# Optimization experiments

Hardware: AMD Instinct MI355X
Metric: run time of the kernel (lower is better)

## Reference

```python
import jax, jax.numpy as jnp
import numpy as np

NUM_HEADS = 16
BLOCK = 64  # block_size = min(64, N)

def setup_inputs() -> dict:
    key = jax.random.key(0)
    k0, k1, k2 = jax.random.split(key, 3)
    B, N, C = 2, 2048, 1024
    x = jax.random.normal(k0, (B, N, C), dtype=jnp.float32)
    w_qkv = jax.random.normal(k1, (3 * C, C), dtype=jnp.float32) * 0.02  # torch Linear weight [out,in]
    w_proj = jax.random.normal(k2, (C, C), dtype=jnp.float32) * 0.02
    b_proj = jnp.zeros((C,), dtype=jnp.float32)
    return {"x": x, "w_qkv": w_qkv, "w_proj": w_proj, "b_proj": b_proj}

def reference(x, w_qkv, w_proj, b_proj):
    B, N, C = x.shape
    H = NUM_HEADS
    hd = C // H
    bs = min(BLOCK, N)
    scale = hd ** -0.5
    # qkv projection: [B,N,3C] -> [3,B,H,N,hd]
    qkv = (x @ w_qkv.T).reshape(B, N, 3, H, hd).transpose(2, 0, 3, 1, 4)
    q, k, v = qkv[0], qkv[1], qkv[2]
    # block-causal mask: query block i attends to all key blocks <= i
    blk = jnp.arange(N) // bs
    mask = blk[:, None] >= blk[None, :]  # [N,N]
    scores = jnp.einsum('bhqd,bhkd->bhqk', q, k) * scale
    scores = jnp.where(mask, scores, -jnp.inf)
    weights = jax.nn.softmax(scores, axis=-1)
    out = jnp.einsum('bhqk,bhkd->bhqd', weights, v)
    out = out.transpose(0, 2, 1, 3).reshape(B, N, C)
    return out @ w_proj.T + b_proj
```

## Files before the change

### kernel.cpp

```cpp
#include <hip/hip_runtime.h>

typedef __attribute__((ext_vector_type(8))) short bf16x8;
typedef __attribute__((ext_vector_type(4))) float f32x4;

__device__ __forceinline__ unsigned short f2bf(float f) {
  unsigned int u = __float_as_uint(f);
  u += 0x7fffu + ((u >> 16) & 1u);
  return (unsigned short)(u >> 16);
}

__device__ __forceinline__ void gload_lds16(const unsigned short* g, unsigned short* l) {
  __builtin_amdgcn_global_load_lds(
      (const __attribute__((address_space(1))) unsigned int*)g,
      (__attribute__((address_space(3))) unsigned int*)l,
      16, 0, 0);
}

__global__ void cvt_bf16_kernel(const float* __restrict__ src,
                                unsigned short* __restrict__ dst, int n) {
  int stride = gridDim.x * blockDim.x;
  for (int i = blockIdx.x * blockDim.x + threadIdx.x; i * 4 < n; i += stride) {
    float4 v = *(const float4*)(src + (size_t)i * 4);
    ushort4 o;
    o.x = f2bf(v.x); o.y = f2bf(v.y); o.z = f2bf(v.z); o.w = f2bf(v.w);
    *(ushort4*)(dst + (size_t)i * 4) = o;
  }
}

__device__ __forceinline__ void gemm128_bt(const unsigned short* __restrict__ A,
                                           const unsigned short* __restrict__ Bt,
                                           unsigned short* As, unsigned short* Bs,
                                           int tm, int tn, f32x4 acc[4][4]) {
  const int K = 1024;
  int tid = threadIdx.x;
  int w = tid >> 6, l = tid & 63;
  int wr = w >> 1, wc = w & 1;
  int g = l >> 4, c = l & 15;

  int srow = w * 32 + (l >> 2);
  int skoff = (l & 3) * 8;
  const unsigned short* gA = A + (size_t)(tm * 128 + srow) * K + skoff;
  const unsigned short* gB = Bt + (size_t)(tn * 128 + srow) * K + skoff;
  unsigned short* lA = As + (w * 32) * 32;
  unsigned short* lB = Bs + (w * 32) * 32;

  for (int k0 = 0; k0 < K; k0 += 32) {
    gload_lds16(gA, lA);
    gload_lds16(gA + 16 * K, lA + 16 * 32);
    gload_lds16(gB, lB);
    gload_lds16(gB + 16 * K, lB + 16 * 32);
    gA += 32; gB += 32;
    __syncthreads();
    bf16x8 af[4], bfr[4];
#pragma unroll
    for (int mi = 0; mi < 4; ++mi)
      af[mi] = *(const bf16x8*)(As + (wr * 64 + mi * 16 + c) * 32 + 8 * g);
#pragma unroll
    for (int ni = 0; ni < 4; ++ni)
      bfr[ni] = *(const bf16x8*)(Bs + (wc * 64 + ni * 16 + c) * 32 + 8 * g);
#pragma unroll
    for (int mi = 0; mi < 4; ++mi)
#pragma unroll
      for (int ni = 0; ni < 4; ++ni)
        acc[mi][ni] = __builtin_amdgcn_mfma_f32_16x16x32_bf16(af[mi], bfr[ni], acc[mi][ni], 0, 0, 0);
    __syncthreads();
  }
}

__global__ __launch_bounds__(256) void qkv_gemm(const unsigned short* __restrict__ xb,
                                                const unsigned short* __restrict__ wb,
                                                unsigned short* __restrict__ Qp,
                                                unsigned short* __restrict__ Kp,
                                                unsigned short* __restrict__ Vt) {
  __shared__ unsigned short As[128 * 32];
  __shared__ unsigned short Bs[128 * 32];
  f32x4 acc[4][4];
#pragma unroll
  for (int i = 0; i < 4; ++i)
#pragma unroll
    for (int j = 0; j < 4; ++j) acc[i][j] = f32x4{0.f, 0.f, 0.f, 0.f};
  int tm = blockIdx.y, tn = blockIdx.x;
  gemm128_bt(xb, wb, As, Bs, tm, tn, acc);

  int tid = threadIdx.x;
  int w = tid >> 6, l = tid & 63;
  int wr = w >> 1, wc = w & 1;
  int g = l >> 4, c = l & 15;
  const float QSCALE = 0.125f * 1.44269504088896f;
#pragma unroll
  for (int mi = 0; mi < 4; ++mi)
#pragma unroll
    for (int ni = 0; ni < 4; ++ni)
#pragma unroll
      for (int r = 0; r < 4; ++r) {
        int row = tm * 128 + wr * 64 + mi * 16 + g * 4 + r;
        int col = tn * 128 + wc * 64 + ni * 16 + c;
        int b = row >> 11, seq = row & 2047;
        int t = col >> 10;
        int h = (col >> 6) & 15, d = col & 63;
        size_t bh = (size_t)b * 16 + h;
        float v = acc[mi][ni][r];
        if (t == 0)      Qp[(bh * 2048 + seq) * 64 + d] = f2bf(v * QSCALE);
        else if (t == 1) Kp[(bh * 2048 + seq) * 64 + d] = f2bf(v);
        else             Vt[(bh * 64 + d) * 2048 + seq] = f2bf(v);
      }
}

__global__ __launch_bounds__(256, 3) void attn_fa(const unsigned short* __restrict__ Qp,
                                                  const unsigned short* __restrict__ Kp,
                                                  const unsigned short* __restrict__ Vt,
                                                  unsigned short* __restrict__ attn) {
  __shared__ unsigned short Ks[2][4096];
  __shared__ unsigned short Vs[2][4096];
  __shared__ unsigned short Plds[4][16][72];
  int tid = threadIdx.x;
  int w = tid >> 6, l = tid & 63;
  int g = l >> 4, c = l & 15;

  int idx = blockIdx.x;
  int pos = idx >> 3;
  int qb = 31 - (pos >> 2);
  int bh = (idx & 7) + 8 * (pos & 3);

  const unsigned short* Qbh = Qp + (size_t)bh * 2048 * 64;
  const unsigned short* Kbh = Kp + (size_t)bh * 2048 * 64;
  const unsigned short* Vbh = Vt + (size_t)bh * 64 * 2048;

  int rowA, colA, rowB, colB;
  { int L = tid * 16;         int P = L ^ (((L >> 7) & 7) << 4); rowA = P >> 7; colA = (P & 127) >> 1; }
  { int L = (tid + 256) * 16; int P = L ^ (((L >> 7) & 7) << 4); rowB = P >> 7; colB = (P & 127) >> 1; }
  const unsigned short* gKA = Kbh + rowA * 64 + colA;
  const unsigned short* gKB = Kbh + rowB * 64 + colB;
  const unsigned short* gVA = Vbh + (size_t)rowA * 2048 + colA;
  const unsigned short* gVB = Vbh + (size_t)rowB * 2048 + colB;

#define STAGE(buf, kb)                                              \
  do {                                                              \
    gload_lds16(gKA + (kb) * 4096, &Ks[(buf)][w * 512]);            \
    gload_lds16(gKB + (kb) * 4096, &Ks[(buf)][w * 512 + 2048]);     \
    gload_lds16(gVA + (kb) * 64,  &Vs[(buf)][w * 512]);             \
    gload_lds16(gVB + (kb) * 64,  &Vs[(buf)][w * 512 + 2048]);      \
  } while (0)

  bf16x8 qf[2];
  {
    size_t qrow = (size_t)qb * 64 + w * 16 + c;
    qf[0] = *(const bf16x8*)(Qbh + qrow * 64 + 8 * g);
    qf[1] = *(const bf16x8*)(Qbh + qrow * 64 + 32 + 8 * g);
  }

  float lp[4] = {0.f, 0.f, 0.f, 0.f};
  f32x4 o[4];
#pragma unroll
  for (int df = 0; df < 4; ++df) o[df] = f32x4{0.f, 0.f, 0.f, 0.f};

  int xorv = c & 7;

  int cur = 0;
  STAGE(0, 0);
  __syncthreads();
  for (int kb = 0; kb <= qb; ++kb) {
    if (kb < qb) STAGE(1 - cur, kb + 1);

    const char* Kb = (const char*)&Ks[cur][0];
    const char* Vb = (const char*)&Vs[cur][0];
    bf16x8 kf[8];
#pragma unroll
    for (int nf = 0; nf < 4; ++nf) {
      int r = nf * 16 + c;
#pragma unroll
      for (int ks = 0; ks < 2; ++ks)
        kf[nf * 2 + ks] = *(const bf16x8*)(Kb + r * 128 + (((ks * 4 + g) ^ xorv) * 16));
    }
    f32x4 s4[4];
#pragma unroll
    for (int nf = 0; nf < 4; ++nf) {
      s4[nf] = f32x4{0.f, 0.f, 0.f, 0.f};
      s4[nf] = __builtin_amdgcn_mfma_f32_16x16x32_bf16(qf[0], kf[nf * 2 + 0], s4[nf], 0, 0, 0);
      s4[nf] = __builtin_amdgcn_mfma_f32_16x16x32_bf16(qf[1], kf[nf * 2 + 1], s4[nf], 0, 0, 0);
    }
    bf16x8 vf[8];
#pragma unroll
    for (int df = 0; df < 4; ++df) {
      int r = df * 16 + c;
#pragma unroll
      for (int ks = 0; ks < 2; ++ks)
        vf[df * 2 + ks] = *(const bf16x8*)(Vb + r * 128 + (((ks * 4 + g) ^ xorv) * 16));
    }
#pragma unroll
    for (int nf = 0; nf < 4; ++nf)
#pragma unroll
      for (int r = 0; r < 4; ++r) {
        float p = __builtin_amdgcn_exp2f(s4[nf][r]);
        lp[r] += p;
        Plds[w][g * 4 + r][nf * 16 + c] = f2bf(p);
      }
#pragma unroll
    for (int ks = 0; ks < 2; ++ks) {
      bf16x8 pf = *(const bf16x8*)(&Plds[w][c][ks * 32 + 8 * g]);
#pragma unroll
      for (int df = 0; df < 4; ++df)
        o[df] = __builtin_amdgcn_mfma_f32_16x16x32_bf16(pf, vf[df * 2 + ks], o[df], 0, 0, 0);
    }
    __syncthreads();
    cur ^= 1;
  }
#undef STAGE

#pragma unroll
  for (int mask = 1; mask < 16; mask <<= 1)
#pragma unroll
    for (int r = 0; r < 4; ++r) lp[r] += __shfl_xor(lp[r], mask);

  int b = bh >> 4, h = bh & 15;
#pragma unroll
  for (int df = 0; df < 4; ++df)
#pragma unroll
    for (int r = 0; r < 4; ++r) {
      int row = qb * 64 + w * 16 + g * 4 + r;
      int colc = h * 64 + df * 16 + c;
      attn[((size_t)b * 2048 + row) * 1024 + colc] = f2bf(o[df][r] / lp[r]);
    }
}

__global__ __launch_bounds__(256) void proj_gemm(const unsigned short* __restrict__ attn,
                                                 const unsigned short* __restrict__ wpb,
                                                 const float* __restrict__ bias,
                                                 float* __restrict__ out) {
  __shared__ unsigned short As[128 * 32];
  __shared__ unsigned short Bs[128 * 32];
  f32x4 acc[4][4];
#pragma unroll
  for (int i = 0; i < 4; ++i)
#pragma unroll
    for (int j = 0; j < 4; ++j) acc[i][j] = f32x4{0.f, 0.f, 0.f, 0.f};
  int tm = blockIdx.y, tn = blockIdx.x;
  gemm128_bt(attn, wpb, As, Bs, tm, tn, acc);

  int tid = threadIdx.x;
  int w = tid >> 6, l = tid & 63;
  int wr = w >> 1, wc = w & 1;
  int g = l >> 4, c = l & 15;
#pragma unroll
  for (int mi = 0; mi < 4; ++mi)
#pragma unroll
    for (int ni = 0; ni < 4; ++ni)
#pragma unroll
      for (int r = 0; r < 4; ++r) {
        int row = tm * 128 + wr * 64 + mi * 16 + g * 4 + r;
        int col = tn * 128 + wc * 64 + ni * 16 + c;
        out[(size_t)row * 1024 + col] = acc[mi][ni][r] + bias[col];
      }
}

extern "C" void kernel_launch(void* const* d_in, const int* in_sizes, int n_in,
                              void* d_out, int out_size, void* d_ws, size_t ws_size,
                              hipStream_t stream) {
  (void)in_sizes; (void)n_in; (void)out_size; (void)ws_size;
  const float* x      = (const float*)d_in[0];
  const float* w_qkv  = (const float*)d_in[1];
  const float* w_proj = (const float*)d_in[2];
  const float* b_proj = (const float*)d_in[3];
  float* out = (float*)d_out;

  unsigned short* xb    = (unsigned short*)d_ws;
  unsigned short* wqkvb = xb + 4096 * 1024;
  unsigned short* wpb   = wqkvb + 3072 * 1024;
  unsigned short* Qp    = wpb + 1024 * 1024;
  unsigned short* Kp    = Qp + 32 * 2048 * 64;
  unsigned short* Vt    = Kp + 32 * 2048 * 64;
  unsigned short* attn  = Vt + 32 * 64 * 2048;

  cvt_bf16_kernel<<<1024, 256, 0, stream>>>(x, xb, 4096 * 1024);
  cvt_bf16_kernel<<<1024, 256, 0, stream>>>(w_qkv, wqkvb, 3072 * 1024);
  cvt_bf16_kernel<<<512, 256, 0, stream>>>(w_proj, wpb, 1024 * 1024);
  qkv_gemm<<<dim3(24, 32), 256, 0, stream>>>(xb, wqkvb, Qp, Kp, Vt);
  attn_fa<<<1024, 256, 0, stream>>>(Qp, Kp, Vt, attn);
  proj_gemm<<<dim3(8, 32), 256, 0, stream>>>(attn, wpb, b_proj, out);
}
```

Baseline: 119.8 us.

## Pipeline GEMM K-loop with 4-stage LDS buffering, XOR swizzle, fused conversion

Replaces the single-buffered GEMM main loop with a 4-stage pipeline of direct global-to-LDS loads. It issues loads three tiles ahead and uses explicit vmcnt waits with a single barrier per iteration. LDS tiles are XOR-swizzled to cut bank conflicts, and MFMA sections run at raised wave priority. The three fp32-to-bf16 conversion launches are merged into one kernel. The cost is 4x the LDS per block and fragile hand-written waitcnt logic.

```diff
diff --git a/kernel.cpp b/kernel.cpp
--- a/kernel.cpp
+++ b/kernel.cpp
@@ -16,71 +16,111 @@
       16, 0, 0);
 }
 
-__global__ void cvt_bf16_kernel(const float* __restrict__ src,
-                                unsigned short* __restrict__ dst, int n) {
+__global__ void cvt_all(const float* __restrict__ x, const float* __restrict__ wq,
+                        const float* __restrict__ wp, unsigned short* __restrict__ dst) {
+  const int n1 = 4096 * 1024 / 4, n2 = 3072 * 1024 / 4, n3 = 1024 * 1024 / 4;
   int stride = gridDim.x * blockDim.x;
-  for (int i = blockIdx.x * blockDim.x + threadIdx.x; i * 4 < n; i += stride) {
-    float4 v = *(const float4*)(src + (size_t)i * 4);
+  for (int i = blockIdx.x * blockDim.x + threadIdx.x; i < n1 + n2 + n3; i += stride) {
+    const float* s; int j;
+    if (i < n1)           { s = x;  j = i; }
+    else if (i < n1 + n2) { s = wq; j = i - n1; }
+    else                  { s = wp; j = i - n1 - n2; }
+    float4 v = ((const float4*)s)[j];
     ushort4 o;
     o.x = f2bf(v.x); o.y = f2bf(v.y); o.z = f2bf(v.z); o.w = f2bf(v.w);
-    *(ushort4*)(dst + (size_t)i * 4) = o;
+    ((ushort4*)dst)[i] = o;
   }
 }
 
-__device__ __forceinline__ void gemm128_bt(const unsigned short* __restrict__ A,
-                                           const unsigned short* __restrict__ Bt,
-                                           unsigned short* As, unsigned short* Bs,
-                                           int tm, int tn, f32x4 acc[4][4]) {
-  const int K = 1024;
+__device__ __forceinline__ void gemm128_pipe(const unsigned short* __restrict__ A,
+                                             const unsigned short* __restrict__ Bt,
+                                             unsigned short* As, unsigned short* Bs,
+                                             int tm, int tn, f32x4 acc[4][4]) {
+  const int K = 1024, NT = 32;
   int tid = threadIdx.x;
   int w = tid >> 6, l = tid & 63;
   int wr = w >> 1, wc = w & 1;
   int g = l >> 4, c = l & 15;
 
-  int srow = w * 32 + (l >> 2);
-  int skoff = (l & 3) * 8;
-  const unsigned short* gA = A + (size_t)(tm * 128 + srow) * K + skoff;
-  const unsigned short* gB = Bt + (size_t)(tn * 128 + srow) * K + skoff;
-  unsigned short* lA = As + (w * 32) * 32;
-  unsigned short* lB = Bs + (w * 32) * 32;
-
-  for (int k0 = 0; k0 < K; k0 += 32) {
-    gload_lds16(gA, lA);
-    gload_lds16(gA + 16 * K, lA + 16 * 32);
-    gload_lds16(gB, lB);
-    gload_lds16(gB + 16 * K, lB + 16 * 32);
-    gA += 32; gB += 32;
-    __syncthreads();
-    bf16x8 af[4], bfr[4];
-#pragma unroll
-    for (int mi = 0; mi < 4; ++mi)
-      af[mi] = *(const bf16x8*)(As + (wr * 64 + mi * 16 + c) * 32 + 8 * g);
-#pragma unroll
-    for (int ni = 0; ni < 4; ++ni)
-      bfr[ni] = *(const bf16x8*)(Bs + (wc * 64 + ni * 16 + c) * 32 + 8 * g);
-#pragma unroll
-    for (int mi = 0; mi < 4; ++mi)
-#pragma unroll
-      for (int ni = 0; ni < 4; ++ni)
-        acc[mi][ni] = __builtin_amdgcn_mfma_f32_16x16x32_bf16(af[mi], bfr[ni], acc[mi][ni], 0, 0, 0);
-    __syncthreads();
+  int L0 = tid * 16;
+  int P0 = L0 ^ (((L0 >> 7) & 7) << 4);
+  int rs = P0 >> 6;
+  int cs = (P0 & 63) >> 1;
+  const unsigned short* gA = A + (size_t)(tm * 128 + rs) * K + cs;
+  const unsigned short* gB = Bt + (size_t)(tn * 128 + rs) * K + cs;
+  unsigned short* lA = As + tid * 8;
+  unsigned short* lB = Bs + tid * 8;
+
+#define STG(t_, s_)                                                  \
+  do {                                                               \
+    const unsigned short* ga_ = gA + (t_) * 32;                      \
+    const unsigned short* gb_ = gB + (t_) * 32;                      \
+    unsigned short* la_ = lA + (s_) * 4096;                          \
+    unsigned short* lb_ = lB + (s_) * 4096;                          \
+    gload_lds16(ga_, la_); gload_lds16(ga_ + 64 * K, la_ + 2048);    \
+    gload_lds16(gb_, lb_); gload_lds16(gb_ + 64 * K, lb_ + 2048);    \
+  } while (0)
+
+  int fx = ((c >> 1) & 7) << 4;
+  int aoff[4], boff[4];
+#pragma unroll
+  for (int mi = 0; mi < 4; ++mi)
+    aoff[mi] = (((wr * 64 + mi * 16 + c) << 6) + (g << 4)) ^ fx;
+#pragma unroll
+  for (int ni = 0; ni < 4; ++ni)
+    boff[ni] = (((wc * 64 + ni * 16 + c) << 6) + (g << 4)) ^ fx;
+
+#define CMP(s_)                                                      \
+  do {                                                               \
+    const char* Ab_ = (const char*)As + (s_) * 8192;                 \
+    const char* Bb_ = (const char*)Bs + (s_) * 8192;                 \
+    bf16x8 af[4], bfv[4];                                            \
+    _Pragma("unroll")                                                \
+    for (int mi = 0; mi < 4; ++mi) af[mi] = *(const bf16x8*)(Ab_ + aoff[mi]); \
+    _Pragma("unroll")                                                \
+    for (int ni = 0; ni < 4; ++ni) bfv[ni] = *(const bf16x8*)(Bb_ + boff[ni]); \
+    __builtin_amdgcn_s_setprio(1);                                   \
+    _Pragma("unroll")                                                \
+    for (int mi = 0; mi < 4; ++mi)                                   \
+      _Pragma("unroll")                                              \
+      for (int ni = 0; ni < 4; ++ni)                                 \
+        acc[mi][ni] = __builtin_amdgcn_mfma_f32_16x16x32_bf16(af[mi], bfv[ni], acc[mi][ni], 0, 0, 0); \
+    __builtin_amdgcn_s_setprio(0);                                   \
+  } while (0)
+
+  STG(0, 0); STG(1, 1); STG(2, 2);
+  asm volatile("s_waitcnt vmcnt(8)" ::: "memory");
+  __builtin_amdgcn_s_barrier();
+
+  for (int t = 0; t < NT; ++t) {
+    if (t + 3 < NT) STG(t + 3, (t + 3) & 3);
+    CMP(t & 3);
+    if (t + 1 < NT) {
+      if (t + 3 < NT)      asm volatile("s_waitcnt vmcnt(8)" ::: "memory");
+      else if (t + 2 < NT) asm volatile("s_waitcnt vmcnt(4)" ::: "memory");
+      else                 asm volatile("s_waitcnt vmcnt(0)" ::: "memory");
+      __builtin_amdgcn_s_barrier();
+      asm volatile("" ::: "memory");
+    }
   }
-}
-
-__global__ __launch_bounds__(256) void qkv_gemm(const unsigned short* __restrict__ xb,
-                                                const unsigned short* __restrict__ wb,
-                                                unsigned short* __restrict__ Qp,
-                                                unsigned short* __restrict__ Kp,
-                                                unsigned short* __restrict__ Vt) {
-  __shared__ unsigned short As[128 * 32];
-  __shared__ unsigned short Bs[128 * 32];
+#undef STG
+#undef CMP
+}
+
+__global__ __launch_bounds__(256, 2) void qkv_gemm(const unsigned short* __restrict__ xb,
+                                                   const unsigned short* __restrict__ wb,
+                                                   unsigned short* __restrict__ Qp,
+                                                   unsigned short* __restrict__ Kp,
+                                                   unsigned short* __restrict__ Vt) {
+  __shared__ unsigned short As[4 * 4096];
+  __shared__ unsigned short Bs[4 * 4096];
   f32x4 acc[4][4];
 #pragma unroll
   for (int i = 0; i < 4; ++i)
 #pragma unroll
     for (int j = 0; j < 4; ++j) acc[i][j] = f32x4{0.f, 0.f, 0.f, 0.f};
   int tm = blockIdx.y, tn = blockIdx.x;
-  gemm128_bt(xb, wb, As, Bs, tm, tn, acc);
+  gemm128_pipe(xb, wb, As, Bs, tm, tn, acc);
 
   int tid = threadIdx.x;
   int w = tid >> 6, l = tid & 63;
@@ -223,19 +263,19 @@
     }
 }
 
-__global__ __launch_bounds__(256) void proj_gemm(const unsigned short* __restrict__ attn,
-                                                 const unsigned short* __restrict__ wpb,
-                                                 const float* __restrict__ bias,
-                                                 float* __restrict__ out) {
-  __shared__ unsigned short As[128 * 32];
-  __shared__ unsigned short Bs[128 * 32];
+__global__ __launch_bounds__(256, 2) void proj_gemm(const unsigned short* __restrict__ attn,
+                                                    const unsigned short* __restrict__ wpb,
+                                                    const float* __restrict__ bias,
+                                                    float* __restrict__ out) {
+  __shared__ unsigned short As[4 * 4096];
+  __shared__ unsigned short Bs[4 * 4096];
   f32x4 acc[4][4];
 #pragma unroll
   for (int i = 0; i < 4; ++i)
 #pragma unroll
     for (int j = 0; j < 4; ++j) acc[i][j] = f32x4{0.f, 0.f, 0.f, 0.f};
   int tm = blockIdx.y, tn = blockIdx.x;
-  gemm128_bt(attn, wpb, As, Bs, tm, tn, acc);
+  gemm128_pipe(attn, wpb, As, Bs, tm, tn, acc);
 
   int tid = threadIdx.x;
   int w = tid >> 6, l = tid & 63;
@@ -271,9 +311,7 @@
   unsigned short* Vt    = Kp + 32 * 2048 * 64;
   unsigned short* attn  = Vt + 32 * 64 * 2048;
 
-  cvt_bf16_kernel<<<1024, 256, 0, stream>>>(x, xb, 4096 * 1024);
-  cvt_bf16_kernel<<<1024, 256, 0, stream>>>(w_qkv, wqkvb, 3072 * 1024);
-  cvt_bf16_kernel<<<512, 256, 0, stream>>>(w_proj, wpb, 1024 * 1024);
+  cvt_all<<<2048, 256, 0, stream>>>(x, w_qkv, w_proj, xb);
   qkv_gemm<<<dim3(24, 32), 256, 0, stream>>>(xb, wqkvb, Qp, Kp, Vt);
   attn_fa<<<1024, 256, 0, stream>>>(Qp, Kp, Vt, attn);
   proj_gemm<<<dim3(8, 32), 256, 0, stream>>>(attn, wpb, b_proj, out);
```

Result: slower. 137.2 us (+14.6%).

## Rewrite QKV GEMM with 256x256 tiles, 4-stage LDS pipeline, merge bf16 conversions

Applied to the files above, without the earlier changes.

The QKV projection GEMM moves from 128x128 tiles with a single LDS buffer to 256x256 tiles run by 512 threads. It uses a 4-stage global-to-LDS prefetch ring with XOR-swizzled LDS addressing, split A/B staging interleaved with MFMA phases, s_setprio, and a swizzled block order for L2 locality. The three fp32-to-bf16 conversion launches are also merged into one kernel. The goal is higher arithmetic intensity, hidden load latency, and fewer launches, at the cost of more registers and LDS per block (128KB), which limits occupancy. The hand-placed vmcnt waits make the pipeline fragile.

```diff
diff --git a/kernel.cpp b/kernel.cpp
--- a/kernel.cpp
+++ b/kernel.cpp
@@ -16,15 +16,126 @@
       16, 0, 0);
 }
 
-__global__ void cvt_bf16_kernel(const float* __restrict__ src,
-                                unsigned short* __restrict__ dst, int n) {
+__global__ void cvt_all(const float* __restrict__ x, const float* __restrict__ wq,
+                        const float* __restrict__ wp, unsigned short* __restrict__ dst) {
+  const int n1 = 4096 * 1024 / 4, n2 = 3072 * 1024 / 4, n3 = 1024 * 1024 / 4;
   int stride = gridDim.x * blockDim.x;
-  for (int i = blockIdx.x * blockDim.x + threadIdx.x; i * 4 < n; i += stride) {
-    float4 v = *(const float4*)(src + (size_t)i * 4);
+  for (int i = blockIdx.x * blockDim.x + threadIdx.x; i < n1 + n2 + n3; i += stride) {
+    const float* s; int j;
+    if (i < n1)           { s = x;  j = i; }
+    else if (i < n1 + n2) { s = wq; j = i - n1; }
+    else                  { s = wp; j = i - n1 - n2; }
+    float4 v = ((const float4*)s)[j];
     ushort4 o;
     o.x = f2bf(v.x); o.y = f2bf(v.y); o.z = f2bf(v.z); o.w = f2bf(v.w);
-    *(ushort4*)(dst + (size_t)i * 4) = o;
-  }
+    ((ushort4*)dst)[i] = o;
+  }
+}
+
+__global__ __launch_bounds__(512, 2) void qkv_gemm(const unsigned short* __restrict__ xb,
+                                                   const unsigned short* __restrict__ wb,
+                                                   unsigned short* __restrict__ Qp,
+                                                   unsigned short* __restrict__ Kp,
+                                                   unsigned short* __restrict__ Vt) {
+  __shared__ unsigned short Lds[4][2][8192];
+  const int K = 1024;
+  int tid = threadIdx.x;
+  int w = tid >> 6, l = tid & 63;
+  int wr = w >> 2, wc = w & 3;
+  int g = l >> 4, c = l & 15;
+
+  int bid = blockIdx.x;
+  int swz = (bid & 7) * 24 + (bid >> 3);
+  int tm = swz / 12, tn = swz - tm * 12;
+
+  int r1 = tid >> 2;
+  int gk = (((tid & 3) ^ ((r1 >> 1) & 3)) << 3);
+  const unsigned short* gA1 = xb + (size_t)(tm * 256 + r1) * K + gk;
+  const unsigned short* gA2 = gA1 + (size_t)128 * K;
+  const unsigned short* gB1 = wb + (size_t)(tn * 256 + r1) * K + gk;
+  const unsigned short* gB2 = gB1 + (size_t)128 * K;
+
+#define STG_A(kt, s) do {                                          \
+    gload_lds16(gA1 + (kt) * 32, &Lds[s][0][tid * 8]);             \
+    gload_lds16(gA2 + (kt) * 32, &Lds[s][0][tid * 8 + 4096]); } while (0)
+#define STG_B(kt, s) do {                                          \
+    gload_lds16(gB1 + (kt) * 32, &Lds[s][1][tid * 8]);             \
+    gload_lds16(gB2 + (kt) * 32, &Lds[s][1][tid * 8 + 4096]); } while (0)
+
+  int fx = (g ^ ((c >> 1) & 3)) << 4;
+  int arow = wr * 128 + c;
+  int brow = wc * 64 + c;
+
+  f32x4 acc[8][4];
+#pragma unroll
+  for (int i = 0; i < 8; ++i)
+#pragma unroll
+    for (int j = 0; j < 4; ++j) acc[i][j] = f32x4{0.f, 0.f, 0.f, 0.f};
+
+  STG_A(0, 0); STG_B(0, 0); STG_A(1, 1); STG_B(1, 1); STG_A(2, 2); STG_B(2, 2);
+  asm volatile("s_waitcnt vmcnt(8)" ::: "memory");
+  __builtin_amdgcn_s_barrier();
+
+  for (int k = 0; k < 32; ++k) {
+    int s = k & 3;
+    const char* Ab = (const char*)&Lds[s][0][0];
+    const char* Bb = (const char*)&Lds[s][1][0];
+    bf16x8 af[4], bfv[4];
+#pragma unroll
+    for (int mi = 0; mi < 4; ++mi)
+      af[mi] = *(const bf16x8*)(Ab + ((arow + mi * 16) << 6) + fx);
+#pragma unroll
+    for (int ni = 0; ni < 4; ++ni)
+      bfv[ni] = *(const bf16x8*)(Bb + ((brow + ni * 16) << 6) + fx);
+    if (k + 3 < 32) STG_A(k + 3, (k + 3) & 3);
+    __builtin_amdgcn_s_barrier();
+    __builtin_amdgcn_s_setprio(1);
+#pragma unroll
+    for (int mi = 0; mi < 4; ++mi)
+#pragma unroll
+      for (int ni = 0; ni < 4; ++ni)
+        acc[mi][ni] = __builtin_amdgcn_mfma_f32_16x16x32_bf16(af[mi], bfv[ni], acc[mi][ni], 0, 0, 0);
+    __builtin_amdgcn_s_setprio(0);
+    __builtin_amdgcn_s_barrier();
+    bf16x8 af2[4];
+#pragma unroll
+    for (int mi = 0; mi < 4; ++mi)
+      af2[mi] = *(const bf16x8*)(Ab + ((arow + (mi + 4) * 16) << 6) + fx);
+    if (k + 3 < 32) STG_B(k + 3, (k + 3) & 3);
+    __builtin_amdgcn_s_barrier();
+    __builtin_amdgcn_s_setprio(1);
+#pragma unroll
+    for (int mi = 0; mi < 4; ++mi)
+#pragma unroll
+      for (int ni = 0; ni < 4; ++ni)
+        acc[mi + 4][ni] = __builtin_amdgcn_mfma_f32_16x16x32_bf16(af2[mi], bfv[ni], acc[mi + 4][ni], 0, 0, 0);
+    __builtin_amdgcn_s_setprio(0);
+    if (k + 3 < 32)      asm volatile("s_waitcnt vmcnt(8)" ::: "memory");
+    else if (k + 2 < 32) asm volatile("s_waitcnt vmcnt(4)" ::: "memory");
+    else if (k + 1 < 32) asm volatile("s_waitcnt vmcnt(0)" ::: "memory");
+    __builtin_amdgcn_s_barrier();
+  }
+#undef STG_A
+#undef STG_B
+
+  const float QSCALE = 0.125f * 1.44269504088896f;
+#pragma unroll
+  for (int mi = 0; mi < 8; ++mi)
+#pragma unroll
+    for (int ni = 0; ni < 4; ++ni)
+#pragma unroll
+      for (int r = 0; r < 4; ++r) {
+        int row = tm * 256 + wr * 128 + mi * 16 + g * 4 + r;
+        int col = tn * 256 + wc * 64 + ni * 16 + c;
+        int b = row >> 11, seq = row & 2047;
+        int ty = col >> 10;
+        int h = (col >> 6) & 15, d = col & 63;
+        size_t bh = (size_t)b * 16 + h;
+        float v = acc[mi][ni][r];
+        if (ty == 0)      Qp[(bh * 2048 + seq) * 64 + d] = f2bf(v * QSCALE);
+        else if (ty == 1) Kp[(bh * 2048 + seq) * 64 + d] = f2bf(v);
+        else              Vt[(bh * 64 + d) * 2048 + seq] = f2bf(v);
+      }
 }
 
 __device__ __forceinline__ void gemm128_bt(const unsigned short* __restrict__ A,
@@ -65,45 +176,6 @@
         acc[mi][ni] = __builtin_amdgcn_mfma_f32_16x16x32_bf16(af[mi], bfr[ni], acc[mi][ni], 0, 0, 0);
     __syncthreads();
   }
-}
-
-__global__ __launch_bounds__(256) void qkv_gemm(const unsigned short* __restrict__ xb,
-                                                const unsigned short* __restrict__ wb,
-                                                unsigned short* __restrict__ Qp,
-                                                unsigned short* __restrict__ Kp,
-                                                unsigned short* __restrict__ Vt) {
-  __shared__ unsigned short As[128 * 32];
-  __shared__ unsigned short Bs[128 * 32];
-  f32x4 acc[4][4];
-#pragma unroll
-  for (int i = 0; i < 4; ++i)
-#pragma unroll
-    for (int j = 0; j < 4; ++j) acc[i][j] = f32x4{0.f, 0.f, 0.f, 0.f};
-  int tm = blockIdx.y, tn = blockIdx.x;
-  gemm128_bt(xb, wb, As, Bs, tm, tn, acc);
-
-  int tid = threadIdx.x;
-  int w = tid >> 6, l = tid & 63;
-  int wr = w >> 1, wc = w & 1;
-  int g = l >> 4, c = l & 15;
-  const float QSCALE = 0.125f * 1.44269504088896f;
-#pragma unroll
-  for (int mi = 0; mi < 4; ++mi)
-#pragma unroll
-    for (int ni = 0; ni < 4; ++ni)
-#pragma unroll
-      for (int r = 0; r < 4; ++r) {
-        int row = tm * 128 + wr * 64 + mi * 16 + g * 4 + r;
-        int col = tn * 128 + wc * 64 + ni * 16 + c;
-        int b = row >> 11, seq = row & 2047;
-        int t = col >> 10;
-        int h = (col >> 6) & 15, d = col & 63;
-        size_t bh = (size_t)b * 16 + h;
-        float v = acc[mi][ni][r];
-        if (t == 0)      Qp[(bh * 2048 + seq) * 64 + d] = f2bf(v * QSCALE);
-        else if (t == 1) Kp[(bh * 2048 + seq) * 64 + d] = f2bf(v);
-        else             Vt[(bh * 64 + d) * 2048 + seq] = f2bf(v);
-      }
 }
 
 __global__ __launch_bounds__(256, 3) void attn_fa(const unsigned short* __restrict__ Qp,
@@ -271,10 +343,8 @@
   unsigned short* Vt    = Kp + 32 * 2048 * 64;
   unsigned short* attn  = Vt + 32 * 64 * 2048;
 
-  cvt_bf16_kernel<<<1024, 256, 0, stream>>>(x, xb, 4096 * 1024);
-  cvt_bf16_kernel<<<1024, 256, 0, stream>>>(w_qkv, wqkvb, 3072 * 1024);
-  cvt_bf16_kernel<<<512, 256, 0, stream>>>(w_proj, wpb, 1024 * 1024);
-  qkv_gemm<<<dim3(24, 32), 256, 0, stream>>>(xb, wqkvb, Qp, Kp, Vt);
+  cvt_all<<<2048, 256, 0, stream>>>(x, w_qkv, w_proj, xb);
+  qkv_gemm<<<192, 512, 0, stream>>>(xb, wqkvb, Qp, Kp, Vt);
   attn_fa<<<1024, 256, 0, stream>>>(Qp, Kp, Vt, attn);
   proj_gemm<<<dim3(8, 32), 256, 0, stream>>>(attn, wpb, b_proj, out);
 }
```

After: 133.4 us. 11.4% more time.

## Widen GEMM K-tile to 64 with XOR-swizzled LDS and fuse bf16 conversions

Applied to the files above, without the earlier changes.

The shared GEMM routine now stages a K=64 slice per iteration instead of 32, using an XOR-swizzled LDS layout to avoid bank conflicts on the fragment reads. This halves the number of barrier pairs per tile and doubles the loads in flight per stage, at the cost of twice the LDS per block. The three fp32-to-bf16 conversion launches are merged into one kernel that writes the contiguous workspace, removing two launches.

```diff
diff --git a/kernel.cpp b/kernel.cpp
--- a/kernel.cpp
+++ b/kernel.cpp
@@ -16,14 +16,19 @@
       16, 0, 0);
 }
 
-__global__ void cvt_bf16_kernel(const float* __restrict__ src,
-                                unsigned short* __restrict__ dst, int n) {
+__global__ void cvt_all(const float* __restrict__ x, const float* __restrict__ wq,
+                        const float* __restrict__ wp, unsigned short* __restrict__ dst) {
+  const int n1 = 4096 * 1024 / 4, n2 = 3072 * 1024 / 4, n3 = 1024 * 1024 / 4;
   int stride = gridDim.x * blockDim.x;
-  for (int i = blockIdx.x * blockDim.x + threadIdx.x; i * 4 < n; i += stride) {
-    float4 v = *(const float4*)(src + (size_t)i * 4);
+  for (int i = blockIdx.x * blockDim.x + threadIdx.x; i < n1 + n2 + n3; i += stride) {
+    const float* s; int j;
+    if (i < n1)           { s = x;  j = i; }
+    else if (i < n1 + n2) { s = wq; j = i - n1; }
+    else                  { s = wp; j = i - n1 - n2; }
+    float4 v = ((const float4*)s)[j];
     ushort4 o;
     o.x = f2bf(v.x); o.y = f2bf(v.y); o.z = f2bf(v.z); o.w = f2bf(v.w);
-    *(ushort4*)(dst + (size_t)i * 4) = o;
+    ((ushort4*)dst)[i] = o;
   }
 }
 
@@ -37,32 +42,43 @@
   int wr = w >> 1, wc = w & 1;
   int g = l >> 4, c = l & 15;
 
-  int srow = w * 32 + (l >> 2);
-  int skoff = (l & 3) * 8;
-  const unsigned short* gA = A + (size_t)(tm * 128 + srow) * K + skoff;
-  const unsigned short* gB = Bt + (size_t)(tn * 128 + srow) * K + skoff;
-  unsigned short* lA = As + (w * 32) * 32;
-  unsigned short* lB = Bs + (w * 32) * 32;
-
-  for (int k0 = 0; k0 < K; k0 += 32) {
+  int r0 = tid >> 3;
+  int ke = (((tid & 7) ^ (r0 & 7)) << 3);
+  const unsigned short* gA = A + (size_t)(tm * 128 + r0) * K + ke;
+  const unsigned short* gB = Bt + (size_t)(tn * 128 + r0) * K + ke;
+  unsigned short* lA = As + tid * 8;
+  unsigned short* lB = Bs + tid * 8;
+
+  int arow = wr * 64 + c;
+  int brow = wc * 64 + c;
+  int cx = c & 7;
+
+  for (int k0 = 0; k0 < K; k0 += 64) {
     gload_lds16(gA, lA);
-    gload_lds16(gA + 16 * K, lA + 16 * 32);
+    gload_lds16(gA + 32 * K, lA + 2048);
+    gload_lds16(gA + 64 * K, lA + 4096);
+    gload_lds16(gA + 96 * K, lA + 6144);
     gload_lds16(gB, lB);
-    gload_lds16(gB + 16 * K, lB + 16 * 32);
-    gA += 32; gB += 32;
+    gload_lds16(gB + 32 * K, lB + 2048);
+    gload_lds16(gB + 64 * K, lB + 4096);
+    gload_lds16(gB + 96 * K, lB + 6144);
+    gA += 64; gB += 64;
     __syncthreads();
-    bf16x8 af[4], bfr[4];
-#pragma unroll
-    for (int mi = 0; mi < 4; ++mi)
-      af[mi] = *(const bf16x8*)(As + (wr * 64 + mi * 16 + c) * 32 + 8 * g);
-#pragma unroll
-    for (int ni = 0; ni < 4; ++ni)
-      bfr[ni] = *(const bf16x8*)(Bs + (wc * 64 + ni * 16 + c) * 32 + 8 * g);
-#pragma unroll
-    for (int mi = 0; mi < 4; ++mi)
+#pragma unroll
+    for (int ks = 0; ks < 2; ++ks) {
+      bf16x8 af[4], bfr[4];
+#pragma unroll
+      for (int mi = 0; mi < 4; ++mi)
+        af[mi] = *(const bf16x8*)((const char*)As + (arow + mi * 16) * 128 + (((ks * 4 + g) ^ cx) << 4));
 #pragma unroll
       for (int ni = 0; ni < 4; ++ni)
-        acc[mi][ni] = __builtin_amdgcn_mfma_f32_16x16x32_bf16(af[mi], bfr[ni], acc[mi][ni], 0, 0, 0);
+        bfr[ni] = *(const bf16x8*)((const char*)Bs + (brow + ni * 16) * 128 + (((ks * 4 + g) ^ cx) << 4));
+#pragma unroll
+      for (int mi = 0; mi < 4; ++mi)
+#pragma unroll
+        for (int ni = 0; ni < 4; ++ni)
+          acc[mi][ni] = __builtin_amdgcn_mfma_f32_16x16x32_bf16(af[mi], bfr[ni], acc[mi][ni], 0, 0, 0);
+    }
     __syncthreads();
   }
 }
@@ -72,8 +88,8 @@
                                                 unsigned short* __restrict__ Qp,
                                                 unsigned short* __restrict__ Kp,
                                                 unsigned short* __restrict__ Vt) {
-  __shared__ unsigned short As[128 * 32];
-  __shared__ unsigned short Bs[128 * 32];
+  __shared__ unsigned short As[128 * 64];
+  __shared__ unsigned short Bs[128 * 64];
   f32x4 acc[4][4];
 #pragma unroll
   for (int i = 0; i < 4; ++i)
@@ -227,8 +243,8 @@
                                                  const unsigned short* __restrict__ wpb,
                                                  const float* __restrict__ bias,
                                                  float* __restrict__ out) {
-  __shared__ unsigned short As[128 * 32];
-  __shared__ unsigned short Bs[128 * 32];
+  __shared__ unsigned short As[128 * 64];
+  __shared__ unsigned short Bs[128 * 64];
   f32x4 acc[4][4];
 #pragma unroll
   for (int i = 0; i < 4; ++i)
@@ -271,9 +287,7 @@
   unsigned short* Vt    = Kp + 32 * 2048 * 64;
   unsigned short* attn  = Vt + 32 * 64 * 2048;
 
-  cvt_bf16_kernel<<<1024, 256, 0, stream>>>(x, xb, 4096 * 1024);
-  cvt_bf16_kernel<<<1024, 256, 0, stream>>>(w_qkv, wqkvb, 3072 * 1024);
-  cvt_bf16_kernel<<<512, 256, 0, stream>>>(w_proj, wpb, 1024 * 1024);
+  cvt_all<<<2048, 256, 0, stream>>>(x, w_qkv, w_proj, xb);
   qkv_gemm<<<dim3(24, 32), 256, 0, stream>>>(xb, wqkvb, Qp, Kp, Vt);
   attn_fa<<<1024, 256, 0, stream>>>(Qp, Kp, Vt, attn);
   proj_gemm<<<dim3(8, 32), 256, 0, stream>>>(attn, wpb, b_proj, out);
```

After: 124.0 us. 3.5% more time.
